# Kernel optimization log

Measured on AMD Instinct MI355X. Metric: run time of the kernel, lower is better.

The kernel has to match this reference:

```python
import jax, jax.numpy as jnp
import numpy as np

DIM = 128
EDGE_COUNT = 128
N_NODES = 128
GRAPH_COUNT = 8
VOCAB = 100000
VEC_DIM = 300


def setup_inputs():
    key = jax.random.key(0)
    ks = jax.random.split(key, 8)
    rng = np.random.default_rng(0)
    data = jnp.asarray(rng.integers(0, VOCAB, size=N_NODES), dtype=jnp.int32)
    types = jnp.zeros((N_NODES,), dtype=jnp.int32)  # single data_type
    edges = jnp.asarray(rng.integers(0, EDGE_COUNT, size=N_NODES), dtype=jnp.int32)
    # parent-offset trees: node i's parent is a node > i, last node is the single root (offset 0)
    g = np.zeros((GRAPH_COUNT, N_NODES), dtype=np.int32)
    for j in range(GRAPH_COUNT):
        for i in range(N_NODES - 1):
            p = int(rng.integers(i + 1, N_NODES))
            g[j, i] = p - i
    graphs = jnp.asarray(g)
    inv_sqrt_d = 1.0 / np.sqrt(DIM)
    inv_sqrt_v = 1.0 / np.sqrt(VEC_DIM)
    return {
        "data": data, "types": types, "graphs": graphs, "edges": edges, "pos": 37,
        "data_vecs": jax.random.normal(ks[0], (VOCAB, VEC_DIM), jnp.float32),
        "data_weights": jax.random.normal(ks[1], (VEC_DIM, DIM), jnp.float32) * inv_sqrt_v,
        "data_biases": jax.random.normal(ks[2], (DIM,), jnp.float32) * 0.1,
        "edge_weights": jax.random.normal(ks[3], (EDGE_COUNT, DIM, DIM), jnp.float32) * inv_sqrt_d,
        "edge_biases": jax.random.normal(ks[4], (EDGE_COUNT, DIM), jnp.float32) * 0.1,
        "score_embedding_weights": jax.random.normal(ks[5], (DIM, 1), jnp.float32) * inv_sqrt_d,
        "score_data_weights": jax.random.normal(ks[6], (DIM, 1), jnp.float32) * inv_sqrt_d,
        "score_bias": jax.random.normal(ks[7], (1, 1), jnp.float32),
    }


def _tree_structure(parents_row):
    # Faithful reproduction of calc_embedding's structure handling (numpy on int constants).
    parents = np.asarray(parents_row).copy()
    n = len(parents)
    roots = [i for i in range(n) if parents[i] == 0]
    for i in range(len(roots) - 1):
        parents[roots[i]] = roots[i + 1]
    root = roots[-1]
    parents[root] = -n
    children = {}
    for i in range(n):
        pp = i + int(parents[i])
        children.setdefault(pp, []).append(i)
    order = []  # DFS preorder from root; reversed gives children-before-parent
    stack = [root]
    while stack:
        node = stack.pop()
        order.append(node)
        stack.extend(children.get(node, []))
    return root, children, order


def _forward(data, types, graphs, edges, pos,
             data_vecs, data_weights, data_biases,
             edge_weights, edge_biases,
             score_embedding_weights, score_data_weights, score_bias):
    data_np = np.asarray(data)
    graphs_np = np.asarray(graphs)
    edges_np = np.asarray(edges).copy()
    E, D, _ = edge_weights.shape
    # data embedding + data score for the queried position
    d_emb = data_vecs[data_np[pos]] @ data_weights + data_biases          # (D,)
    d_score = score_bias[0, 0] + d_emb @ score_data_weights[:, 0]         # scalar
    edges_np[pos] = -1  # unknown edge at pos -> branch over all edge types
    # base embeddings for all nodes at once: (N, D)
    base = data_vecs[data_np] @ data_weights + data_biases

    def transform(child_emb, eid):
        # child_emb: (E, D). eid < 0 -> per-edge-type weights (baddbmm over all E edges)
        if eid < 0:
            return jnp.einsum('ed,edk->ek', child_emb, edge_weights) + edge_biases
        return child_emb @ edge_weights[eid] + edge_biases[eid]

    scores = []
    for j in range(graphs_np.shape[0]):
        root, children, order = _tree_structure(graphs_np[j])
        emb = {}
        for n in reversed(order):  # children before parents
            e = jnp.broadcast_to(base[n], (E, D))
            ch = children.get(n, [])
            for c in ch:
                e = e + transform(emb.pop(c), int(edges_np[c]))
            if ch:
                e = jax.nn.relu(e)  # clamp(min=0) only for internal nodes
            emb[n] = e
        res = transform(emb[root], int(edges_np[root]))  # add_child_embedding(zeros, root_emb, edges[root])
        scores.append(d_score + res @ score_embedding_weights[:, 0])  # (E,)
    return jnp.stack(scores)  # (GRAPH_COUNT, EDGE_COUNT)


def reference(data, types, graphs, edges, pos, data_vecs, data_weights, data_biases,
              edge_weights, edge_biases, score_embedding_weights, score_data_weights, score_bias):
    return _forward(data, types, graphs, edges, pos, data_vecs, data_weights, data_biases,
                    edge_weights, edge_biases, score_embedding_weights, score_data_weights, score_bias)
```

## Files before the change

### kernel.cpp

```cpp
#include <hip/hip_runtime.h>
#include <stdint.h>


#define NND 128
#define DD  128
#define GG  8
#define VD  300
#define CH  4

typedef unsigned int u32;

#define F_POS  (1<<16)
#define F_PATH (1<<17)

__global__ void __launch_bounds__(128) k_base(
        const int* __restrict__ data, const int* __restrict__ posArr,
        const float* __restrict__ vecs, const float* __restrict__ dw,
        const float* __restrict__ db,   const float* __restrict__ sdw,
        const float* __restrict__ sb,
        float* __restrict__ base, float* __restrict__ dscore)
{
    __shared__ __align__(16) float row[VD];
    __shared__ float red[DD];
    int n = blockIdx.x, t = threadIdx.x;
    int id = data[n];
    const float4* vp = (const float4*)(vecs + (size_t)id * VD);
    for (int i = t; i < VD/4; i += 128) ((float4*)row)[i] = vp[i];
    __syncthreads();
    float a0 = db[t], a1 = 0.f, a2 = 0.f, a3 = 0.f;
    for (int d = 0; d < VD; d += 4){
        a0 = fmaf(row[d+0], dw[(d+0)*DD + t], a0);
        a1 = fmaf(row[d+1], dw[(d+1)*DD + t], a1);
        a2 = fmaf(row[d+2], dw[(d+2)*DD + t], a2);
        a3 = fmaf(row[d+3], dw[(d+3)*DD + t], a3);
    }
    float acc = (a0 + a1) + (a2 + a3);
    base[n*DD + t] = acc;
    if (n == posArr[0]){
        red[t] = acc * sdw[t];
        __syncthreads();
        for (int o = 64; o > 0; o >>= 1){ if (t < o) red[t] += red[t+o]; __syncthreads(); }
        if (t == 0) dscore[0] = sb[0] + red[0];
    }
}

__global__ void __launch_bounds__(1024, 1) k_tree(
        const int* __restrict__ graphs, const int* __restrict__ edges,
        const int* __restrict__ posArr, const float* __restrict__ EW,
        const float* __restrict__ EB,   const float* __restrict__ base,
        float* __restrict__ vposG, float* __restrict__ uG, int* __restrict__ meta)
{
    __shared__ __align__(16) float contrib[NND-1][DD];
    __shared__ int par_s[NND], eid_s[NND], flg_s[NND];
    __shared__ int ccnt[NND], cstart[NND], cidx[NND];
    __shared__ int dep[NND], anc[NND], lcnt[NND], lstart[NND], order[NND];
    __shared__ int maxD_s;

    int g = blockIdx.x, t = threadIdx.x;

    if (t < NND){
        par_s[t] = (t < NND-1) ? (t + graphs[g*NND + t]) : (NND-1);
        eid_s[t] = edges[t];
        flg_s[t] = 0;
        ccnt[t]  = 0;
        lcnt[t]  = 0;
    }
    if (t == 0) maxD_s = 0;
    __syncthreads();

    int mySlot = 0;
    if (t < NND-1){
        int p = par_s[t];
        atomicAdd(&ccnt[p], 1);
        for (int c = 0; c < t; ++c) mySlot += (par_s[c] == p);
    }
    if (t < NND){
        dep[t] = (t < NND-1) ? 1 : 0;
        anc[t] = par_s[t];
    }
    if (t == 0){
        int p = posArr[0];
        flg_s[p] |= F_POS;
        int c = par_s[p], s = 0;
        for (;;){
            flg_s[c] |= F_PATH | (s << 24);
            meta[g*(NND+1) + 1 + s] = c;
            ++s;
            if (c == NND-1) break;
            c = par_s[c];
        }
        meta[g*(NND+1)] = s;
    }
    __syncthreads();

    if (t < NND){
        int s = 0;
        for (int p = 0; p < t; ++p) s += ccnt[p];
        cstart[t] = s;
    }
    __syncthreads();
    if (t < NND-1) cidx[cstart[par_s[t]] + mySlot] = t;

    for (int k = 0; k < 7; ++k){
        int d2 = 0, a2 = 0;
        if (t < NND){ d2 = dep[t] + dep[anc[t]]; a2 = anc[anc[t]]; }
        __syncthreads();
        if (t < NND){ dep[t] = d2; anc[t] = a2; }
        __syncthreads();
    }
    if (t < NND) atomicMax(&maxD_s, dep[t]);
    if (t < NND) atomicAdd(&lcnt[dep[t]], 1);
    __syncthreads();

    if (t < NND){
        int s = 0;
        for (int d2 = 0; d2 < t; ++d2) s += lcnt[d2];
        lstart[t] = s;
    }
    __syncthreads();
    if (t < NND){
        int d2 = dep[t], s = 0;
        for (int c = 0; c < t; ++c) s += (dep[c] == d2);
        order[lstart[d2] + s] = t;
    }
    __syncthreads();

    int w = t >> 6, l = t & 63;
    int c0 = 2*l;
    int maxD = maxD_s;

    for (int d = maxD; d >= 0; --d){
        int lo = lstart[d], cnt = lcnt[d];
        for (int q = w; q < cnt; q += 16){
            int n = order[lo + q];
            float2 bse = *(const float2*)&base[n*DD + c0];
            float e0 = bse.x, e1 = bse.y;
            int cs = cstart[n], cc = ccnt[n];
            for (int j = 0; j < cc; ++j){
                int c = cidx[cs + j];
                if (!(flg_s[c] & (F_POS | F_PATH))){
                    float2 cv = *(const float2*)&contrib[c][c0];
                    e0 += cv.x; e1 += cv.y;
                }
            }
            int f = flg_s[n];
            if (f & F_POS){
                if (cc){ e0 = fmaxf(e0, 0.f); e1 = fmaxf(e1, 0.f); }
                *(float2*)&vposG[g*DD + c0] = make_float2(e0, e1);
            } else if (f & F_PATH){
                int slot = ((u32)f) >> 24;
                *(float2*)&uG[((size_t)g*NND + slot)*DD + c0] = make_float2(e0, e1);
            } else {
                if (cc){ e0 = fmaxf(e0, 0.f); e1 = fmaxf(e1, 0.f); }
                *(float2*)&contrib[n][c0] = make_float2(e0, e1);
                asm volatile("s_waitcnt lgkmcnt(0)" ::: "memory");
                int e = eid_s[n];
                const float* Wp = EW + (size_t)e*(DD*DD) + c0;
                float s0a=0.f, s1a=0.f, s0b=0.f, s1b=0.f;
                #pragma unroll 8
                for (int dd = 0; dd < DD/2; ++dd){
                    float x0 = contrib[n][dd];
                    float x1 = contrib[n][DD/2 + dd];
                    float2 w0 = *(const float2*)&Wp[(size_t)dd*DD];
                    float2 w1 = *(const float2*)&Wp[(size_t)(DD/2+dd)*DD];
                    s0a = fmaf(x0, w0.x, s0a); s1a = fmaf(x0, w0.y, s1a);
                    s0b = fmaf(x1, w1.x, s0b); s1b = fmaf(x1, w1.y, s1b);
                }
                float2 bb = *(const float2*)&EB[(size_t)e*DD + c0];
                *(float2*)&contrib[n][c0] = make_float2(s0a + s0b + bb.x,
                                                        s1a + s1b + bb.y);
            }
        }
        __syncthreads();
    }
}

__global__ void __launch_bounds__(256, 1) k_chain(
        const int* __restrict__ edges,
        const float* __restrict__ EW, const float* __restrict__ EB,
        const float* __restrict__ SEW,
        const float* __restrict__ vposG, const float* __restrict__ uG,
        const int* __restrict__ meta, const float* __restrict__ dscore,
        float* __restrict__ outp)
{
    __shared__ __align__(16) float Vbuf[2][CH][DD];
    __shared__ float red[CH][4];
    int g = blockIdx.x >> 5, chunk = blockIdx.x & 31;
    int t = threadIdx.x, l = t & 63, w = t >> 6;
    int k4 = w*8 + (l & 7);
    int d0 = (l >> 3) * 16;
    bool owner = ((l >> 3) == 0);
    int eBase = chunk * CH;
    int L = meta[g*(NND+1)];

    float vpf[16];
    #pragma unroll
    for (int j = 0; j < 4; ++j){
        float4 x = *(const float4*)&vposG[g*DD + d0 + 4*j];
        vpf[4*j+0]=x.x; vpf[4*j+1]=x.y; vpf[4*j+2]=x.z; vpf[4*j+3]=x.w;
    }
    float4 u0 = *(const float4*)&uG[(size_t)g*NND*DD + 4*k4];

    #pragma unroll 2
    for (int p = 0; p < CH; ++p){
        int e = eBase + p;
        const float* Wp = EW + (size_t)e*(DD*DD) + (size_t)d0*DD + 4*k4;
        float s0=0.f, s1=0.f, s2=0.f, s3=0.f;
        #pragma unroll
        for (int d = 0; d < 16; ++d){
            float4 wv = *(const float4*)&Wp[d*DD];
            s0 = fmaf(vpf[d], wv.x, s0);
            s1 = fmaf(vpf[d], wv.y, s1);
            s2 = fmaf(vpf[d], wv.z, s2);
            s3 = fmaf(vpf[d], wv.w, s3);
        }
        #pragma unroll
        for (int m = 8; m <= 32; m <<= 1){
            s0 += __shfl_xor(s0, m); s1 += __shfl_xor(s1, m);
            s2 += __shfl_xor(s2, m); s3 += __shfl_xor(s3, m);
        }
        if (owner){
            float4 bb = *(const float4*)&EB[(size_t)e*DD + 4*k4];
            float4 r;
            r.x = fmaxf(u0.x + s0 + bb.x, 0.f);
            r.y = fmaxf(u0.y + s1 + bb.y, 0.f);
            r.z = fmaxf(u0.z + s2 + bb.z, 0.f);
            r.w = fmaxf(u0.w + s3 + bb.w, 0.f);
            *(float4*)&Vbuf[0][p][4*k4] = r;
        }
    }
    __syncthreads();

    int cur = 0;
    for (int s = 1; s < L; ++s){
        int pn = meta[g*(NND+1) + s];
        int ej = edges[pn];
        const float* Wp = EW + (size_t)ej*(DD*DD) + (size_t)d0*DD + 4*k4;
        float4 wr[16];
        #pragma unroll
        for (int d = 0; d < 16; ++d) wr[d] = *(const float4*)&Wp[d*DD];
        float4 us = *(const float4*)&uG[((size_t)g*NND + s)*DD + 4*k4];
        float4 bb = *(const float4*)&EB[(size_t)ej*DD + 4*k4];
        #pragma unroll
        for (int p = 0; p < CH; ++p){
            float ev[16];
            #pragma unroll
            for (int j = 0; j < 4; ++j){
                float4 x = *(const float4*)&Vbuf[cur][p][d0 + 4*j];
                ev[4*j+0]=x.x; ev[4*j+1]=x.y; ev[4*j+2]=x.z; ev[4*j+3]=x.w;
            }
            float s0=0.f, s1=0.f, s2=0.f, s3=0.f;
            #pragma unroll
            for (int d = 0; d < 16; ++d){
                s0 = fmaf(ev[d], wr[d].x, s0);
                s1 = fmaf(ev[d], wr[d].y, s1);
                s2 = fmaf(ev[d], wr[d].z, s2);
                s3 = fmaf(ev[d], wr[d].w, s3);
            }
            #pragma unroll
            for (int m = 8; m <= 32; m <<= 1){
                s0 += __shfl_xor(s0, m); s1 += __shfl_xor(s1, m);
                s2 += __shfl_xor(s2, m); s3 += __shfl_xor(s3, m);
            }
            if (owner){
                float4 r;
                r.x = fmaxf(us.x + s0 + bb.x, 0.f);
                r.y = fmaxf(us.y + s1 + bb.y, 0.f);
                r.z = fmaxf(us.z + s2 + bb.z, 0.f);
                r.w = fmaxf(us.w + s3 + bb.w, 0.f);
                *(float4*)&Vbuf[cur^1][p][4*k4] = r;
            }
        }
        __syncthreads();
        cur ^= 1;
    }

    {
        int rn = meta[g*(NND+1) + L];
        int er = edges[rn];
        const float* Wp = EW + (size_t)er*(DD*DD) + (size_t)d0*DD + 4*k4;
        float4 wr[16];
        #pragma unroll
        for (int d = 0; d < 16; ++d) wr[d] = *(const float4*)&Wp[d*DD];
        float4 bb = *(const float4*)&EB[(size_t)er*DD + 4*k4];
        float4 sw = *(const float4*)&SEW[4*k4];
        #pragma unroll
        for (int p = 0; p < CH; ++p){
            float ev[16];
            #pragma unroll
            for (int j = 0; j < 4; ++j){
                float4 x = *(const float4*)&Vbuf[cur][p][d0 + 4*j];
                ev[4*j+0]=x.x; ev[4*j+1]=x.y; ev[4*j+2]=x.z; ev[4*j+3]=x.w;
            }
            float s0=0.f, s1=0.f, s2=0.f, s3=0.f;
            #pragma unroll
            for (int d = 0; d < 16; ++d){
                s0 = fmaf(ev[d], wr[d].x, s0);
                s1 = fmaf(ev[d], wr[d].y, s1);
                s2 = fmaf(ev[d], wr[d].z, s2);
                s3 = fmaf(ev[d], wr[d].w, s3);
            }
            #pragma unroll
            for (int m = 8; m <= 32; m <<= 1){
                s0 += __shfl_xor(s0, m); s1 += __shfl_xor(s1, m);
                s2 += __shfl_xor(s2, m); s3 += __shfl_xor(s3, m);
            }
            if (owner){
                float part = (s0 + bb.x) * sw.x + (s1 + bb.y) * sw.y
                           + (s2 + bb.z) * sw.z + (s3 + bb.w) * sw.w;
                part += __shfl_xor(part, 1);
                part += __shfl_xor(part, 2);
                part += __shfl_xor(part, 4);
                if (l == 0) red[p][w] = part;
            }
        }
        __syncthreads();
        if (t < CH)
            outp[g*DD + eBase + t] = dscore[0] + red[t][0] + red[t][1] + red[t][2] + red[t][3];
    }
}

extern "C" void kernel_launch(void* const* d_in, const int* in_sizes, int n_in,
                              void* d_out, int out_size, void* d_ws, size_t ws_size,
                              hipStream_t stream)
{
    const int*   data   = (const int*)d_in[0];
    const int*   graphs = (const int*)d_in[2];
    const int*   edges  = (const int*)d_in[3];
    const int*   posArr = (const int*)d_in[4];
    const float* vecs   = (const float*)d_in[5];
    const float* dw     = (const float*)d_in[6];
    const float* db     = (const float*)d_in[7];
    const float* ew     = (const float*)d_in[8];
    const float* eb     = (const float*)d_in[9];
    const float* sew    = (const float*)d_in[10];
    const float* sdw    = (const float*)d_in[11];
    const float* sb     = (const float*)d_in[12];

    char* ws = (char*)d_ws;
    float* base   = (float*)(ws);
    float* vposG  = (float*)(ws + 65536);
    float* uG     = (float*)(ws + 65536 + 4096);
    float* dscore = (float*)(ws + 65536 + 4096 + 524288);
    int*   meta   = (int*)  (ws + 65536 + 4096 + 524288 + 256);

    float* outp = (float*)d_out;

    k_base <<<NND, 128, 0, stream>>>(data, posArr, vecs, dw, db, sdw, sb, base, dscore);
    k_tree <<<GG, 1024, 0, stream>>>(graphs, edges, posArr, ew, eb, base, vposG, uG, meta);
    k_chain<<<GG*(DD/CH), 256, 0, stream>>>(edges, ew, eb, sew, vposG, uG, meta, dscore, outp);
}
```

Baseline: 356.2 us.

## Split chain kernel into per-edge first step and wider-chunk path steps

The chain kernel is split in two. A new k_step0 kernel runs one block per edge: it loads that edge's weight matrix once and applies it to all graphs, writing the first-step vectors to workspace. The path-step kernel then handles 16 edges per block instead of 4, so each path-node weight tile is reused across more columns and far fewer blocks reload the same weights. Separately, the tree matvec is rewritten with float4 double-buffered weight loads split across two half-waves. The cost is an extra launch, a workspace round trip, and only 64 blocks in the serial path phase, which may leave the GPU under-occupied.

```diff
diff --git a/kernel.cpp b/kernel.cpp
--- a/kernel.cpp
+++ b/kernel.cpp
@@ -6,7 +6,8 @@
 #define DD  128
 #define GG  8
 #define VD  300
-#define CH  4
+#define EDGEN 128
+#define CH2 16
 
 typedef unsigned int u32;
 
@@ -127,6 +128,8 @@
 
     int w = t >> 6, l = t & 63;
     int c0 = 2*l;
+    int li = l & 31, hl = l >> 5;
+    int c4 = 4*li, dbase = 64*hl;
     int maxD = maxD_s;
 
     for (int d = maxD; d >= 0; --d){
@@ -155,64 +158,73 @@
                 *(float2*)&contrib[n][c0] = make_float2(e0, e1);
                 asm volatile("s_waitcnt lgkmcnt(0)" ::: "memory");
                 int e = eid_s[n];
-                const float* Wp = EW + (size_t)e*(DD*DD) + c0;
-                float s0a=0.f, s1a=0.f, s0b=0.f, s1b=0.f;
-                #pragma unroll 8
-                for (int dd = 0; dd < DD/2; ++dd){
-                    float x0 = contrib[n][dd];
-                    float x1 = contrib[n][DD/2 + dd];
-                    float2 w0 = *(const float2*)&Wp[(size_t)dd*DD];
-                    float2 w1 = *(const float2*)&Wp[(size_t)(DD/2+dd)*DD];
-                    s0a = fmaf(x0, w0.x, s0a); s1a = fmaf(x0, w0.y, s1a);
-                    s0b = fmaf(x1, w1.x, s0b); s1b = fmaf(x1, w1.y, s1b);
+                const float* Wp = EW + (size_t)e*(DD*DD) + (size_t)dbase*DD + c4;
+                const float* xr = &contrib[n][dbase];
+                float4 A[8], B[8];
+                float s0=0.f, s1=0.f, s2=0.f, s3=0.f;
+                #define LW(buf, gi) { _Pragma("unroll") \
+                    for (int j2 = 0; j2 < 8; ++j2) \
+                        buf[j2] = *(const float4*)&Wp[(size_t)((gi)*8 + j2)*DD]; }
+                #define CP(buf, gi) { _Pragma("unroll") \
+                    for (int j2 = 0; j2 < 8; ++j2){ \
+                        float x = xr[(gi)*8 + j2]; \
+                        s0 = fmaf(x, buf[j2].x, s0); s1 = fmaf(x, buf[j2].y, s1); \
+                        s2 = fmaf(x, buf[j2].z, s2); s3 = fmaf(x, buf[j2].w, s3); } }
+                LW(A,0); LW(B,1);
+                CP(A,0); LW(A,2);
+                CP(B,1); LW(B,3);
+                CP(A,2); LW(A,4);
+                CP(B,3); LW(B,5);
+                CP(A,4); LW(A,6);
+                CP(B,5); LW(B,7);
+                CP(A,6);
+                CP(B,7);
+                #undef LW
+                #undef CP
+                s0 += __shfl_xor(s0, 32);
+                s1 += __shfl_xor(s1, 32);
+                s2 += __shfl_xor(s2, 32);
+                s3 += __shfl_xor(s3, 32);
+                if (hl == 0){
+                    float4 bb = *(const float4*)&EB[(size_t)e*DD + c4];
+                    *(float4*)&contrib[n][c4] =
+                        make_float4(s0 + bb.x, s1 + bb.y, s2 + bb.z, s3 + bb.w);
                 }
-                float2 bb = *(const float2*)&EB[(size_t)e*DD + c0];
-                *(float2*)&contrib[n][c0] = make_float2(s0a + s0b + bb.x,
-                                                        s1a + s1b + bb.y);
-            }
-        }
-        __syncthreads();
-    }
-}
-
-__global__ void __launch_bounds__(256, 1) k_chain(
-        const int* __restrict__ edges,
+            }
+        }
+        __syncthreads();
+    }
+}
+
+__global__ void __launch_bounds__(256, 1) k_step0(
         const float* __restrict__ EW, const float* __restrict__ EB,
-        const float* __restrict__ SEW,
         const float* __restrict__ vposG, const float* __restrict__ uG,
-        const int* __restrict__ meta, const float* __restrict__ dscore,
-        float* __restrict__ outp)
-{
-    __shared__ __align__(16) float Vbuf[2][CH][DD];
-    __shared__ float red[CH][4];
-    int g = blockIdx.x >> 5, chunk = blockIdx.x & 31;
-    int t = threadIdx.x, l = t & 63, w = t >> 6;
+        float* __restrict__ V0)
+{
+    __shared__ __align__(16) float vpos_s[GG][DD];
+    int e = blockIdx.x, t = threadIdx.x, l = t & 63, w = t >> 6;
+    {
+        int idx = t;
+        ((float4*)vpos_s)[idx] = ((const float4*)vposG)[idx];
+    }
+    __syncthreads();
     int k4 = w*8 + (l & 7);
     int d0 = (l >> 3) * 16;
     bool owner = ((l >> 3) == 0);
-    int eBase = chunk * CH;
-    int L = meta[g*(NND+1)];
-
-    float vpf[16];
+    const float* Wp = EW + (size_t)e*(DD*DD) + (size_t)d0*DD + 4*k4;
+    float4 wr[16];
     #pragma unroll
-    for (int j = 0; j < 4; ++j){
-        float4 x = *(const float4*)&vposG[g*DD + d0 + 4*j];
-        vpf[4*j+0]=x.x; vpf[4*j+1]=x.y; vpf[4*j+2]=x.z; vpf[4*j+3]=x.w;
-    }
-    float4 u0 = *(const float4*)&uG[(size_t)g*NND*DD + 4*k4];
-
-    #pragma unroll 2
-    for (int p = 0; p < CH; ++p){
-        int e = eBase + p;
-        const float* Wp = EW + (size_t)e*(DD*DD) + (size_t)d0*DD + 4*k4;
+    for (int d = 0; d < 16; ++d) wr[d] = *(const float4*)&Wp[d*DD];
+    float4 bb = *(const float4*)&EB[(size_t)e*DD + 4*k4];
+    for (int g = 0; g < GG; ++g){
         float s0=0.f, s1=0.f, s2=0.f, s3=0.f;
         #pragma unroll
         for (int d = 0; d < 16; ++d){
-            float4 wv = *(const float4*)&Wp[d*DD];
-            s0 = fmaf(vpf[d], wv.x, s0);
-            s1 = fmaf(vpf[d], wv.y, s1);
-            s2 = fmaf(vpf[d], wv.z, s2);
-            s3 = fmaf(vpf[d], wv.w, s3);
+            float x = vpos_s[g][d0 + d];
+            s0 = fmaf(x, wr[d].x, s0);
+            s1 = fmaf(x, wr[d].y, s1);
+            s2 = fmaf(x, wr[d].z, s2);
+            s3 = fmaf(x, wr[d].w, s3);
         }
         #pragma unroll
         for (int m = 8; m <= 32; m <<= 1){
@@ -220,15 +232,38 @@
             s2 += __shfl_xor(s2, m); s3 += __shfl_xor(s3, m);
         }
         if (owner){
-            float4 bb = *(const float4*)&EB[(size_t)e*DD + 4*k4];
+            float4 u0 = *(const float4*)&uG[(size_t)g*NND*DD + 4*k4];
             float4 r;
             r.x = fmaxf(u0.x + s0 + bb.x, 0.f);
             r.y = fmaxf(u0.y + s1 + bb.y, 0.f);
             r.z = fmaxf(u0.z + s2 + bb.z, 0.f);
             r.w = fmaxf(u0.w + s3 + bb.w, 0.f);
-            *(float4*)&Vbuf[0][p][4*k4] = r;
-        }
-    }
+            *(float4*)&V0[((size_t)g*EDGEN + e)*DD + 4*k4] = r;
+        }
+    }
+}
+
+__global__ void __launch_bounds__(256, 1) k_steps(
+        const int* __restrict__ edges,
+        const float* __restrict__ EW, const float* __restrict__ EB,
+        const float* __restrict__ SEW,
+        const float* __restrict__ uG, const float* __restrict__ V0,
+        const int* __restrict__ meta, const float* __restrict__ dscore,
+        float* __restrict__ outp)
+{
+    __shared__ __align__(16) float Vbuf[2][CH2][DD];
+    __shared__ float red[CH2][4];
+    int g = blockIdx.x >> 3, chunk = blockIdx.x & 7;
+    int t = threadIdx.x, l = t & 63, w = t >> 6;
+    int k4 = w*8 + (l & 7);
+    int d0 = (l >> 3) * 16;
+    bool owner = ((l >> 3) == 0);
+    int eBase = chunk * CH2;
+    int L = meta[g*(NND+1)];
+
+    for (int idx = t; idx < CH2*DD/4; idx += 256)
+        ((float4*)&Vbuf[0][0][0])[idx] =
+            ((const float4*)&V0[((size_t)g*EDGEN + eBase)*DD])[idx];
     __syncthreads();
 
     int cur = 0;
@@ -241,8 +276,8 @@
         for (int d = 0; d < 16; ++d) wr[d] = *(const float4*)&Wp[d*DD];
         float4 us = *(const float4*)&uG[((size_t)g*NND + s)*DD + 4*k4];
         float4 bb = *(const float4*)&EB[(size_t)ej*DD + 4*k4];
-        #pragma unroll
-        for (int p = 0; p < CH; ++p){
+        #pragma unroll 4
+        for (int p = 0; p < CH2; ++p){
             float ev[16];
             #pragma unroll
             for (int j = 0; j < 4; ++j){
@@ -284,8 +319,8 @@
         for (int d = 0; d < 16; ++d) wr[d] = *(const float4*)&Wp[d*DD];
         float4 bb = *(const float4*)&EB[(size_t)er*DD + 4*k4];
         float4 sw = *(const float4*)&SEW[4*k4];
-        #pragma unroll
-        for (int p = 0; p < CH; ++p){
+        #pragma unroll 4
+        for (int p = 0; p < CH2; ++p){
             float ev[16];
             #pragma unroll
             for (int j = 0; j < 4; ++j){
@@ -315,7 +350,7 @@
             }
         }
         __syncthreads();
-        if (t < CH)
+        if (t < CH2)
             outp[g*DD + eBase + t] = dscore[0] + red[t][0] + red[t][1] + red[t][2] + red[t][3];
     }
 }
@@ -341,12 +376,14 @@
     float* base   = (float*)(ws);
     float* vposG  = (float*)(ws + 65536);
     float* uG     = (float*)(ws + 65536 + 4096);
-    float* dscore = (float*)(ws + 65536 + 4096 + 524288);
-    int*   meta   = (int*)  (ws + 65536 + 4096 + 524288 + 256);
+    float* dscore = (float*)(ws + 593920);
+    int*   meta   = (int*)  (ws + 594176);
+    float* V0     = (float*)(ws + 598528);
 
     float* outp = (float*)d_out;
 
     k_base <<<NND, 128, 0, stream>>>(data, posArr, vecs, dw, db, sdw, sb, base, dscore);
     k_tree <<<GG, 1024, 0, stream>>>(graphs, edges, posArr, ew, eb, base, vposG, uG, meta);
-    k_chain<<<GG*(DD/CH), 256, 0, stream>>>(edges, ew, eb, sew, vposG, uG, meta, dscore, outp);
-}
+    k_step0<<<EDGEN, 256, 0, stream>>>(ew, eb, vposG, uG, V0);
+    k_steps<<<GG*(EDGEN/CH2), 256, 0, stream>>>(edges, ew, eb, sew, uG, V0, meta, dscore, outp);
+}
```

After: 345.8 us. 2.9% less time.
